# Optimization experiments

Measured on AMD Instinct MI355X. Metric: run time of the kernel, lower is better.

The kernel has to match this reference:

```python
import jax, jax.numpy as jnp
import numpy as np

INPUT_DIM, K, L, D_C = 512, 3, 512, 64
LN_EPS = 1e-5
NORM_EPS = 1e-12


def setup_inputs() -> dict:
    key = jax.random.key(0)
    ks = jax.random.split(key, 16)
    s = 0.02
    inp = {
        "x": jax.random.normal(ks[0], (65536, INPUT_DIM), jnp.float32),
        # per-sub-encoder MLP weights, stacked over K
        "W1": jax.random.normal(ks[1], (K, INPUT_DIM, 256), jnp.float32) * s,
        "b1": jnp.zeros((K, 256), jnp.float32),
        "W2": jax.random.normal(ks[2], (K, 256, 128), jnp.float32) * s,
        "b2": jnp.zeros((K, 128), jnp.float32),
        "W3": jax.random.normal(ks[3], (K, 128, D_C), jnp.float32) * s,
        "b3": jnp.zeros((K, D_C), jnp.float32),
        # shared output LayerNorm
        "gamma": jnp.ones((D_C,), jnp.float32),
        "beta": jnp.zeros((D_C,), jnp.float32),
        # codebooks: nn.Parameter(torch.randn(L, d_c)) per sub-quantizer
        "codebooks": jax.random.normal(ks[4], (K, L, D_C), jnp.float32),
        # decoder MLP d_c -> 128 -> 256 -> input_dim
        "D1": jax.random.normal(ks[5], (D_C, 128), jnp.float32) * s,
        "c1": jnp.zeros((128,), jnp.float32),
        "D2": jax.random.normal(ks[6], (128, 256), jnp.float32) * s,
        "c2": jnp.zeros((256,), jnp.float32),
        "D3": jax.random.normal(ks[7], (256, INPUT_DIM), jnp.float32) * s,
        "c3": jnp.zeros((INPUT_DIM,), jnp.float32),
    }
    return inp


def _l2norm(v, axis=-1):
    # F.normalize(p=2): x / max(||x||, eps)
    n = jnp.sqrt(jnp.sum(v * v, axis=axis, keepdims=True))
    return v / jnp.maximum(n, NORM_EPS)


def reference(x, W1, b1, W2, b2, W3, b3, gamma, beta, codebooks,
              D1, c1, D2, c2, D3, c3):
    sg = jax.lax.stop_gradient
    # encode all K sub-encoders in one batched einsum: (K, B, *)
    h = jax.nn.relu(jnp.einsum('bi,kio->kbo', x, W1) + b1[:, None, :])
    h = jax.nn.relu(jnp.einsum('kbo,kop->kbp', h, W2) + b2[:, None, :])
    enc = jnp.einsum('kbp,kpd->kbd', h, W3) + b3[:, None, :]  # (K,B,d_c)
    # LayerNorm over d_c
    mu = jnp.mean(enc, axis=-1, keepdims=True)
    var = jnp.mean((enc - mu) ** 2, axis=-1, keepdims=True)
    enc = (enc - mu) * jax.lax.rsqrt(var + LN_EPS) * gamma + beta
    # cosine quantize
    enc_n = _l2norm(enc)
    cb_n = _l2norm(codebooks)                       # (K,L,d_c)
    cos = jnp.einsum('kbd,kld->kbl', enc_n, cb_n)   # (K,B,L)
    idx = jnp.argmax(cos, axis=-1)                  # argmin(1-cos) == argmax(cos), (K,B)
    q = jnp.take_along_axis(cb_n, idx[:, :, None], axis=1)  # (K,B,d_c)
    # straight-through
    q_ste = enc + sg(q - enc)
    codebook_loss = jnp.sum(jnp.mean((sg(enc) - q_ste) ** 2, axis=(1, 2)))
    commitment_loss = jnp.sum(jnp.mean((enc - sg(q_ste)) ** 2, axis=(1, 2)))
    avg_q = jnp.mean(q_ste, axis=0)                 # (B,d_c)
    h = jax.nn.relu(avg_q @ D1 + c1)
    h = jax.nn.relu(h @ D2 + c2)
    reconstructed = h @ D3 + c3                     # (B,input_dim)
    recon_loss = jnp.mean((reconstructed - x) ** 2)
    tokens = idx.T                                  # (B,K)
    return tokens, reconstructed, recon_loss, codebook_loss, commitment_loss
```

## Files before the change

### kernel.cpp

```cpp
#include <hip/hip_runtime.h>
#include <hip/hip_bf16.h>

using f4 = float4;
typedef __attribute__((ext_vector_type(8))) short bf16x8;
typedef __attribute__((ext_vector_type(4))) float f32x4;

constexpr int IN_DIM = 512;
constexpr int DC     = 64;
constexpr int LCB    = 512;

__device__ __forceinline__ float wave_sum64(float v) {
#pragma unroll
    for (int m = 1; m < 64; m <<= 1) v += __shfl_xor(v, m, 64);
    return v;
}

__device__ __forceinline__ unsigned short f2bf(float v) {
    __hip_bfloat16 h = __float2bfloat16(v);
    return *(unsigned short*)&h;
}

__global__ void cbnorm_kernel(const float* __restrict__ cb, float* __restrict__ cbn,
                              float* __restrict__ cbnT, float* __restrict__ accv) {
    int row  = blockIdx.x * 4 + (threadIdx.x >> 6);
    int lane = threadIdx.x & 63;
    float v  = cb[(size_t)row * DC + lane];
    float ss = wave_sum64(v * v);
    float n  = sqrtf(ss);
    float o  = v / fmaxf(n, 1e-12f);
    cbn[(size_t)row * DC + lane] = o;
    int k = row >> 9, l = row & 511;
    cbnT[((size_t)k * DC + lane) * LCB + l] = o;
    if (blockIdx.x == 0 && threadIdx.x < 16) accv[threadIdx.x] = 0.f;
}

__global__ void wcvt_kernel(const float* __restrict__ D1, const float* __restrict__ D2,
                            const float* __restrict__ D3, unsigned short* __restrict__ D1t,
                            unsigned short* __restrict__ D2t, unsigned short* __restrict__ D3t) {
    int i = blockIdx.x * 256 + threadIdx.x;
    if (i < 128 * 64)  { int n = i >> 6, k = i & 63;  D1t[i] = f2bf(D1[(size_t)k * 128 + n]); }
    if (i < 256 * 128) { int n = i >> 7, k = i & 127; D2t[i] = f2bf(D2[(size_t)k * 256 + n]); }
    if (i < 512 * 256) { int n = i >> 8, k = i & 255; D3t[i] = f2bf(D3[(size_t)k * 512 + n]); }
}

__global__ void avgq_kernel(const float* __restrict__ q3, unsigned short* __restrict__ Aq,
                            int n4, size_t planeStride) {
    int i = blockIdx.x * blockDim.x + threadIdx.x;
    if (i >= n4) return;
    f4 a = *(const f4*)&q3[(size_t)i * 4];
    f4 b = *(const f4*)&q3[planeStride + (size_t)i * 4];
    f4 c = *(const f4*)&q3[2 * planeStride + (size_t)i * 4];
    const float s = 1.f / 3.f;
    unsigned int lo = f2bf((a.x + b.x + c.x) * s) | ((unsigned int)f2bf((a.y + b.y + c.y) * s) << 16);
    unsigned int hi = f2bf((a.z + b.z + c.z) * s) | ((unsigned int)f2bf((a.w + b.w + c.w) * s) << 16);
    uint2 o; o.x = lo; o.y = hi;
    *(uint2*)&Aq[(size_t)i * 4] = o;
}

template <int RELU>
__global__ __launch_bounds__(256, 4)
void gemm_kernel(const float* __restrict__ A, const float* __restrict__ W,
                 const float* __restrict__ bias, float* __restrict__ C,
                 int Kin, int N,
                 size_t aK, size_t wK, size_t bK, size_t cK) {
    constexpr int BM = 128, BN = 128, BK = 32;
    __shared__ alignas(16) float As[BK][BM + 4];
    __shared__ alignas(16) float Ws[BK][BN + 4];
    const int z = blockIdx.z;
    A += (size_t)z * aK;  W += (size_t)z * wK;
    bias += (size_t)z * bK;  C += (size_t)z * cK;
    const int tid = threadIdx.x;
    const int tx = tid & 15, ty = tid >> 4;
    const int row0 = blockIdx.x * BM, col0 = blockIdx.y * BN;

    float acc[8][8];
#pragma unroll
    for (int i = 0; i < 8; i++)
#pragma unroll
        for (int j = 0; j < 8; j++) acc[i][j] = 0.f;

    const int aRow = tid >> 3;
    const int aCol = (tid & 7) * 4;
    const int wRow = tid >> 5;
    const int wCol = (tid & 31) * 4;

    for (int kk = 0; kk < Kin; kk += BK) {
#pragma unroll
        for (int it = 0; it < 4; it++) {
            f4 v = *(const f4*)&A[(size_t)(row0 + aRow + it * 32) * Kin + kk + aCol];
            As[aCol + 0][aRow + it * 32] = v.x;
            As[aCol + 1][aRow + it * 32] = v.y;
            As[aCol + 2][aRow + it * 32] = v.z;
            As[aCol + 3][aRow + it * 32] = v.w;
        }
#pragma unroll
        for (int it = 0; it < 4; it++) {
            f4 v = *(const f4*)&W[(size_t)(kk + wRow + it * 8) * N + col0 + wCol];
            *(f4*)&Ws[wRow + it * 8][wCol] = v;
        }
        __syncthreads();
#pragma unroll
        for (int p = 0; p < BK; p++) {
            f4 a0 = *(const f4*)&As[p][ty * 8];
            f4 a1 = *(const f4*)&As[p][ty * 8 + 4];
            f4 w0 = *(const f4*)&Ws[p][tx * 8];
            f4 w1 = *(const f4*)&Ws[p][tx * 8 + 4];
            float av[8] = {a0.x, a0.y, a0.z, a0.w, a1.x, a1.y, a1.z, a1.w};
            float wv[8] = {w0.x, w0.y, w0.z, w0.w, w1.x, w1.y, w1.z, w1.w};
#pragma unroll
            for (int i = 0; i < 8; i++)
#pragma unroll
                for (int j = 0; j < 8; j++)
                    acc[i][j] = fmaf(av[i], wv[j], acc[i][j]);
        }
        __syncthreads();
    }

#pragma unroll
    for (int i = 0; i < 8; i++) {
        const size_t r = (size_t)row0 + ty * 8 + i;
        float vrow[8];
#pragma unroll
        for (int j = 0; j < 8; j++) {
            float v = acc[i][j] + bias[col0 + tx * 8 + j];
            if (RELU) v = fmaxf(v, 0.f);
            vrow[j] = v;
        }
        *(f4*)&C[r * N + col0 + tx * 8]     = *(f4*)&vrow[0];
        *(f4*)&C[r * N + col0 + tx * 8 + 4] = *(f4*)&vrow[4];
    }
}

__global__ __launch_bounds__(256, 4)
void gemm_ln_kernel(const float* __restrict__ A, const float* __restrict__ W,
                    const float* __restrict__ bias, const float* __restrict__ gamma,
                    const float* __restrict__ beta, float* __restrict__ enc, int Kin,
                    size_t aK, size_t wK, size_t bK, size_t eK) {
    constexpr int BM = 128, BK = 32;
    __shared__ alignas(16) float As[BK][BM + 4];
    __shared__ alignas(16) float Ws[BK][DC + 4];
    const int z = blockIdx.y;
    A += (size_t)z * aK;  W += (size_t)z * wK;
    bias += (size_t)z * bK;  enc += (size_t)z * eK;
    const int tid = threadIdx.x;
    const int tx = tid & 7, ty = tid >> 3;
    const int row0 = blockIdx.x * BM;

    float acc[4][8];
#pragma unroll
    for (int i = 0; i < 4; i++)
#pragma unroll
        for (int j = 0; j < 8; j++) acc[i][j] = 0.f;

    const int aRow = tid >> 3;
    const int aCol = (tid & 7) * 4;
    const int wRow = tid >> 4;
    const int wCol = (tid & 15) * 4;

    for (int kk = 0; kk < Kin; kk += BK) {
#pragma unroll
        for (int it = 0; it < 4; it++) {
            f4 v = *(const f4*)&A[(size_t)(row0 + aRow + it * 32) * Kin + kk + aCol];
            As[aCol + 0][aRow + it * 32] = v.x;
            As[aCol + 1][aRow + it * 32] = v.y;
            As[aCol + 2][aRow + it * 32] = v.z;
            As[aCol + 3][aRow + it * 32] = v.w;
        }
#pragma unroll
        for (int it = 0; it < 2; it++) {
            f4 v = *(const f4*)&W[(size_t)(kk + wRow + it * 16) * DC + wCol];
            *(f4*)&Ws[wRow + it * 16][wCol] = v;
        }
        __syncthreads();
#pragma unroll
        for (int p = 0; p < BK; p++) {
            f4 a  = *(const f4*)&As[p][ty * 4];
            f4 w0 = *(const f4*)&Ws[p][tx * 8];
            f4 w1 = *(const f4*)&Ws[p][tx * 8 + 4];
            float av[4] = {a.x, a.y, a.z, a.w};
            float wv[8] = {w0.x, w0.y, w0.z, w0.w, w1.x, w1.y, w1.z, w1.w};
#pragma unroll
            for (int i = 0; i < 4; i++)
#pragma unroll
                for (int j = 0; j < 8; j++)
                    acc[i][j] = fmaf(av[i], wv[j], acc[i][j]);
        }
        __syncthreads();
    }

#pragma unroll
    for (int i = 0; i < 4; i++) {
        float vrow[8];
#pragma unroll
        for (int j = 0; j < 8; j++) vrow[j] = acc[i][j] + bias[tx * 8 + j];
        float s = 0.f;
#pragma unroll
        for (int j = 0; j < 8; j++) s += vrow[j];
#pragma unroll
        for (int m = 1; m < 8; m <<= 1) s += __shfl_xor(s, m, 8);
        float mu = s * (1.f / 64.f);
        float d2 = 0.f;
#pragma unroll
        for (int j = 0; j < 8; j++) { float d = vrow[j] - mu; d2 = fmaf(d, d, d2); }
#pragma unroll
        for (int m = 1; m < 8; m <<= 1) d2 += __shfl_xor(d2, m, 8);
        float rs = 1.f / sqrtf(d2 * (1.f / 64.f) + 1e-5f);
#pragma unroll
        for (int j = 0; j < 8; j++) {
            int c = tx * 8 + j;
            vrow[j] = (vrow[j] - mu) * rs * gamma[c] + beta[c];
        }
        const size_t r = (size_t)row0 + ty * 4 + i;
        *(f4*)&enc[r * DC + tx * 8]     = *(f4*)&vrow[0];
        *(f4*)&enc[r * DC + tx * 8 + 4] = *(f4*)&vrow[4];
    }
}

__global__ __launch_bounds__(256, 2)
void quant_kernel(float* __restrict__ enc, const float* __restrict__ cbT,
                  const float* __restrict__ cbn, float* __restrict__ out_tok,
                  float* __restrict__ sse_acc, int row_off_glob,
                  size_t eK, size_t cbTK, size_t cbnK) {
    constexpr int BM = 128;
    __shared__ alignas(16) float Es[DC][BM + 4];
    __shared__ alignas(16) float Cs[DC][64 + 4];
    __shared__ float red[4];
    const int k = blockIdx.y;
    enc += (size_t)k * eK;
    cbT += (size_t)k * cbTK;
    cbn += (size_t)k * cbnK;
    const int tid = threadIdx.x;
    const int tx = tid & 7, ty = tid >> 3;
    const int row0 = blockIdx.x * BM;

    {
        const int r  = tid >> 1;
        const int c0 = (tid & 1) * 32;
#pragma unroll
        for (int i = 0; i < 8; i++) {
            f4 v = *(const f4*)&enc[(size_t)(row0 + r) * DC + c0 + i * 4];
            Es[c0 + i * 4 + 0][r] = v.x;
            Es[c0 + i * 4 + 1][r] = v.y;
            Es[c0 + i * 4 + 2][r] = v.z;
            Es[c0 + i * 4 + 3][r] = v.w;
        }
    }

    double mx[4]; int mi[4];
#pragma unroll
    for (int i = 0; i < 4; i++) { mx[i] = -1.0e300; mi[i] = 0; }

    for (int lc = 0; lc < LCB; lc += 64) {
        __syncthreads();
        {
            const int p  = tid >> 2;
            const int c0 = (tid & 3) * 16;
#pragma unroll
            for (int i = 0; i < 4; i++)
                *(f4*)&Cs[p][c0 + i * 4] =
                    *(const f4*)&cbT[(size_t)p * LCB + lc + c0 + i * 4];
        }
        __syncthreads();
        double sc[4][8];
#pragma unroll
        for (int i = 0; i < 4; i++)
#pragma unroll
            for (int j = 0; j < 8; j++) sc[i][j] = 0.0;
#pragma unroll
        for (int p = 0; p < DC; p++) {
            f4 a  = *(const f4*)&Es[p][ty * 4];
            f4 w0 = *(const f4*)&Cs[p][tx * 8];
            f4 w1 = *(const f4*)&Cs[p][tx * 8 + 4];
            double av[4] = {a.x, a.y, a.z, a.w};
            double wv[8] = {w0.x, w0.y, w0.z, w0.w, w1.x, w1.y, w1.z, w1.w};
#pragma unroll
            for (int i = 0; i < 4; i++)
#pragma unroll
                for (int j = 0; j < 8; j++)
                    sc[i][j] = fma(av[i], wv[j], sc[i][j]);
        }
#pragma unroll
        for (int i = 0; i < 4; i++)
#pragma unroll
            for (int j = 0; j < 8; j++) {
                int l = lc + tx * 8 + j;
                if (sc[i][j] > mx[i]) { mx[i] = sc[i][j]; mi[i] = l; }
            }
    }

#pragma unroll
    for (int m = 1; m < 8; m <<= 1)
#pragma unroll
        for (int i = 0; i < 4; i++) {
            double omx = __shfl_xor(mx[i], m, 8);
            int    omi = __shfl_xor(mi[i], m, 8);
            if (omx > mx[i] || (omx == mx[i] && omi < mi[i])) { mx[i] = omx; mi[i] = omi; }
        }

    float sse = 0.f;
#pragma unroll
    for (int i = 0; i < 4; i++) {
        const int rl = ty * 4 + i;
        const size_t r = (size_t)row0 + rl;
        f4 q0 = *(const f4*)&cbn[(size_t)mi[i] * DC + tx * 8];
        f4 q1 = *(const f4*)&cbn[(size_t)mi[i] * DC + tx * 8 + 4];
        float qv[8] = {q0.x, q0.y, q0.z, q0.w, q1.x, q1.y, q1.z, q1.w};
#pragma unroll
        for (int j = 0; j < 8; j++) {
            float e = Es[tx * 8 + j][rl];
            float d = e - qv[j];
            sse = fmaf(d, d, sse);
        }
        *(f4*)&enc[r * DC + tx * 8]     = q0;
        *(f4*)&enc[r * DC + tx * 8 + 4] = q1;
        if (tx == 0) out_tok[(size_t)(row_off_glob + r) * 3 + k] = (float)mi[i];
    }
    sse = wave_sum64(sse);
    if ((tid & 63) == 0) red[tid >> 6] = sse;
    __syncthreads();
    if (tid == 0) atomicAdd(sse_acc, red[0] + red[1] + red[2] + red[3]);
}

template <int RELU, int FINAL>
__global__ __launch_bounds__(256, 2)
void mfma_dec_kernel(const unsigned short* __restrict__ A,
                     const unsigned short* __restrict__ Wt,
                     const float* __restrict__ bias,
                     unsigned short* __restrict__ Cb, float* __restrict__ Cf,
                     const float* __restrict__ x, float* __restrict__ sse_acc,
                     int Kin, int N) {
    constexpr int BM = 128, BN = 128, BK = 32;
    __shared__ alignas(16) unsigned short As[BM][BK + 8];
    __shared__ alignas(16) unsigned short Ws[BN][BK + 8];
    __shared__ float red[4];
    const int tid = threadIdx.x;
    const int l = tid & 63, wave = tid >> 6;
    const int wr = wave >> 1, wc = wave & 1;
    const int row0 = blockIdx.x * BM, col0 = blockIdx.y * BN;

    f32x4 acc[4][4];
#pragma unroll
    for (int m = 0; m < 4; m++)
#pragma unroll
        for (int n = 0; n < 4; n++) acc[m][n] = (f32x4){0.f, 0.f, 0.f, 0.f};

    const int sRow = tid >> 1;
    const int sCol = (tid & 1) * 16;

    for (int kt = 0; kt < Kin; kt += BK) {
        __syncthreads();
        {
            uint4 a0 = *(const uint4*)&A[(size_t)(row0 + sRow) * Kin + kt + sCol];
            uint4 a1 = *(const uint4*)&A[(size_t)(row0 + sRow) * Kin + kt + sCol + 8];
            uint4 w0 = *(const uint4*)&Wt[(size_t)(col0 + sRow) * Kin + kt + sCol];
            uint4 w1 = *(const uint4*)&Wt[(size_t)(col0 + sRow) * Kin + kt + sCol + 8];
            *(uint4*)&As[sRow][sCol]     = a0;
            *(uint4*)&As[sRow][sCol + 8] = a1;
            *(uint4*)&Ws[sRow][sCol]     = w0;
            *(uint4*)&Ws[sRow][sCol + 8] = w1;
        }
        __syncthreads();
        bf16x8 af[4], bf[4];
        const int k0 = (l >> 4) * 8;
        const int lr = l & 15;
#pragma unroll
        for (int m = 0; m < 4; m++)
            af[m] = *(const bf16x8*)&As[wr * 64 + m * 16 + lr][k0];
#pragma unroll
        for (int n = 0; n < 4; n++)
            bf[n] = *(const bf16x8*)&Ws[wc * 64 + n * 16 + lr][k0];
#pragma unroll
        for (int m = 0; m < 4; m++)
#pragma unroll
            for (int n = 0; n < 4; n++)
                acc[m][n] = __builtin_amdgcn_mfma_f32_16x16x32_bf16(af[m], bf[n], acc[m][n], 0, 0, 0);
    }

    float sse = 0.f;
#pragma unroll
    for (int m = 0; m < 4; m++)
#pragma unroll
        for (int n = 0; n < 4; n++) {
            const int rbase = row0 + wr * 64 + m * 16 + (l >> 4) * 4;
            const int c = col0 + wc * 64 + n * 16 + (l & 15);
            const float b = bias[c];
#pragma unroll
            for (int rr = 0; rr < 4; rr++) {
                float v = acc[m][n][rr] + b;
                if (FINAL) {
                    float d = v - x[(size_t)(rbase + rr) * N + c];
                    sse = fmaf(d, d, sse);
                    Cf[(size_t)(rbase + rr) * N + c] = v;
                } else {
                    if (RELU) v = fmaxf(v, 0.f);
                    Cb[(size_t)(rbase + rr) * N + c] = f2bf(v);
                }
            }
        }
    if (FINAL) {
        sse = wave_sum64(sse);
        if ((tid & 63) == 0) red[tid >> 6] = sse;
        __syncthreads();
        if (tid == 0) atomicAdd(sse_acc, red[0] + red[1] + red[2] + red[3]);
    }
}

__global__ void finalize_kernel(const float* __restrict__ accv,
                                float* __restrict__ outs,
                                float inv_rec, float inv_cb) {
    if (threadIdx.x == 0) {
        outs[0] = accv[1] * inv_rec;
        float cbl = accv[0] * inv_cb;
        outs[1] = cbl;
        outs[2] = cbl;
    }
}

extern "C" void kernel_launch(void* const* d_in, const int* in_sizes, int n_in,
                              void* d_out, int out_size, void* d_ws, size_t ws_size,
                              hipStream_t stream) {
    const float* x     = (const float*)d_in[0];
    const float* W1    = (const float*)d_in[1];
    const float* b1    = (const float*)d_in[2];
    const float* W2    = (const float*)d_in[3];
    const float* b2    = (const float*)d_in[4];
    const float* W3    = (const float*)d_in[5];
    const float* b3    = (const float*)d_in[6];
    const float* gamma = (const float*)d_in[7];
    const float* beta  = (const float*)d_in[8];
    const float* cb    = (const float*)d_in[9];
    const float* D1    = (const float*)d_in[10];
    const float* c1    = (const float*)d_in[11];
    const float* D2    = (const float*)d_in[12];
    const float* c2    = (const float*)d_in[13];
    const float* D3    = (const float*)d_in[14];
    const float* c3    = (const float*)d_in[15];
    const int M = in_sizes[0] / IN_DIM;

    float* out     = (float*)d_out;
    float* out_tok = out;
    float* out_rec = out + (size_t)M * 3;
    float* out_sc  = out_rec + (size_t)M * IN_DIM;

    const size_t fixedB  = (size_t)(16 + 2 * 3 * LCB * DC) * 4 + (size_t)172032 * 2;
    const size_t perRowB = (size_t)(3 * DC + 3 * 256 + 3 * 128) * 4;
    int C = 4096;
    for (int cand = 65536; cand >= 4096; cand >>= 1)
        if (fixedB + (size_t)cand * perRowB <= ws_size) { C = cand; break; }

    float* ws    = (float*)d_ws;
    float* accv  = ws;
    float* cbn   = accv + 16;
    float* cbnT  = cbn + 3 * LCB * DC;
    unsigned short* D1t = (unsigned short*)(cbnT + 3 * DC * LCB);
    unsigned short* D2t = D1t + 128 * 64;
    unsigned short* D3t = D2t + 256 * 128;
    float* enc3  = (float*)(D3t + 512 * 256);
    float* H1    = enc3 + (size_t)3 * C * DC;
    float* H2    = H1 + (size_t)3 * C * 256;
    unsigned short* Aq  = (unsigned short*)H2;
    unsigned short* H1b = Aq + (size_t)C * 64;
    unsigned short* H2b = H1b + (size_t)C * 128;

    cbnorm_kernel<<<dim3(3 * LCB / 4), dim3(256), 0, stream>>>(cb, cbn, cbnT, accv);
    wcvt_kernel<<<dim3(512), dim3(256), 0, stream>>>(D1, D2, D3, D1t, D2t, D3t);

    for (int off = 0; off < M; off += C) {
        const float* xc  = x + (size_t)off * IN_DIM;
        float*       rcc = out_rec + (size_t)off * IN_DIM;

        gemm_kernel<1><<<dim3(C / 128, 2, 3), dim3(256), 0, stream>>>(
            xc, W1, b1, H1, 512, 256,
            0, (size_t)512 * 256, 256, (size_t)C * 256);
        gemm_kernel<1><<<dim3(C / 128, 1, 3), dim3(256), 0, stream>>>(
            H1, W2, b2, H2, 256, 128,
            (size_t)C * 256, (size_t)256 * 128, 128, (size_t)C * 128);
        gemm_ln_kernel<<<dim3(C / 128, 3), dim3(256), 0, stream>>>(
            H2, W3, b3, gamma, beta, enc3, 128,
            (size_t)C * 128, (size_t)128 * 64, 64, (size_t)C * DC);
        quant_kernel<<<dim3(C / 128, 3), dim3(256), 0, stream>>>(
            enc3, cbnT, cbn, out_tok, accv + 0, off,
            (size_t)C * DC, (size_t)DC * LCB, (size_t)LCB * DC);

        avgq_kernel<<<dim3((C * 16 + 255) / 256), dim3(256), 0, stream>>>(
            enc3, Aq, C * 16, (size_t)C * DC);
        mfma_dec_kernel<1, 0><<<dim3(C / 128, 1), dim3(256), 0, stream>>>(
            Aq, D1t, c1, H1b, nullptr, nullptr, nullptr, 64, 128);
        mfma_dec_kernel<1, 0><<<dim3(C / 128, 2), dim3(256), 0, stream>>>(
            H1b, D2t, c2, H2b, nullptr, nullptr, nullptr, 128, 256);
        mfma_dec_kernel<0, 1><<<dim3(C / 128, 4), dim3(256), 0, stream>>>(
            H2b, D3t, c3, nullptr, rcc, xc, accv + 1, 256, 512);
    }

    finalize_kernel<<<dim3(1), dim3(64), 0, stream>>>(
        accv, out_sc, 1.f / ((float)M * IN_DIM), 1.f / ((float)M * DC));
}
```

Baseline: 1.234 ms.

## Fuse encoder layer-2 GEMM into LayerNorm GEMM and prewiden codebook tile to double

```diff
diff --git a/kernel.cpp b/kernel.cpp
--- a/kernel.cpp
+++ b/kernel.cpp
@@ -132,55 +132,65 @@
 }
 
 __global__ __launch_bounds__(256, 4)
-void gemm_ln_kernel(const float* __restrict__ A, const float* __restrict__ W,
-                    const float* __restrict__ bias, const float* __restrict__ gamma,
-                    const float* __restrict__ beta, float* __restrict__ enc, int Kin,
-                    size_t aK, size_t wK, size_t bK, size_t eK) {
-    constexpr int BM = 128, BK = 32;
-    __shared__ alignas(16) float As[BK][BM + 4];
-    __shared__ alignas(16) float Ws[BK][DC + 4];
+void gemm2_ln_kernel(const float* __restrict__ A, const float* __restrict__ W2,
+                     const float* __restrict__ b2, const float* __restrict__ W3,
+                     const float* __restrict__ b3, const float* __restrict__ gamma,
+                     const float* __restrict__ beta, float* __restrict__ enc,
+                     size_t aK, size_t w2K, size_t b2K, size_t w3K, size_t b3K,
+                     size_t eK) {
+    constexpr int BM = 128, BN = 128, BK = 32, KIN = 256;
+    __shared__ union SM {
+        struct { alignas(16) float As[BK][BM + 4]; alignas(16) float Ws[BK][BN + 4]; } a;
+        struct { alignas(16) float Hs[128][66]; } b;
+    } sm;
     const int z = blockIdx.y;
-    A += (size_t)z * aK;  W += (size_t)z * wK;
-    bias += (size_t)z * bK;  enc += (size_t)z * eK;
+    A += (size_t)z * aK;
+    const float* W2p = W2 + (size_t)z * w2K;
+    const float* b2p = b2 + (size_t)z * b2K;
+    const float* W3p = W3 + (size_t)z * w3K;
+    const float* b3p = b3 + (size_t)z * b3K;
+    float* encp = enc + (size_t)z * eK;
+
     const int tid = threadIdx.x;
-    const int tx = tid & 7, ty = tid >> 3;
+    const int tx = tid & 15, ty = tid >> 4;
     const int row0 = blockIdx.x * BM;
 
-    float acc[4][8];
-#pragma unroll
-    for (int i = 0; i < 4; i++)
+    float acc[8][8];
+#pragma unroll
+    for (int i = 0; i < 8; i++)
 #pragma unroll
         for (int j = 0; j < 8; j++) acc[i][j] = 0.f;
 
     const int aRow = tid >> 3;
     const int aCol = (tid & 7) * 4;
-    const int wRow = tid >> 4;
-    const int wCol = (tid & 15) * 4;
-
-    for (int kk = 0; kk < Kin; kk += BK) {
+    const int wRow = tid >> 5;
+    const int wCol = (tid & 31) * 4;
+
+    for (int kk = 0; kk < KIN; kk += BK) {
 #pragma unroll
         for (int it = 0; it < 4; it++) {
-            f4 v = *(const f4*)&A[(size_t)(row0 + aRow + it * 32) * Kin + kk + aCol];
-            As[aCol + 0][aRow + it * 32] = v.x;
-            As[aCol + 1][aRow + it * 32] = v.y;
-            As[aCol + 2][aRow + it * 32] = v.z;
-            As[aCol + 3][aRow + it * 32] = v.w;
-        }
-#pragma unroll
-        for (int it = 0; it < 2; it++) {
-            f4 v = *(const f4*)&W[(size_t)(kk + wRow + it * 16) * DC + wCol];
-            *(f4*)&Ws[wRow + it * 16][wCol] = v;
+            f4 v = *(const f4*)&A[(size_t)(row0 + aRow + it * 32) * KIN + kk + aCol];
+            sm.a.As[aCol + 0][aRow + it * 32] = v.x;
+            sm.a.As[aCol + 1][aRow + it * 32] = v.y;
+            sm.a.As[aCol + 2][aRow + it * 32] = v.z;
+            sm.a.As[aCol + 3][aRow + it * 32] = v.w;
+        }
+#pragma unroll
+        for (int it = 0; it < 4; it++) {
+            f4 v = *(const f4*)&W2p[(size_t)(kk + wRow + it * 8) * BN + wCol];
+            *(f4*)&sm.a.Ws[wRow + it * 8][wCol] = v;
         }
         __syncthreads();
 #pragma unroll
         for (int p = 0; p < BK; p++) {
-            f4 a  = *(const f4*)&As[p][ty * 4];
-            f4 w0 = *(const f4*)&Ws[p][tx * 8];
-            f4 w1 = *(const f4*)&Ws[p][tx * 8 + 4];
-            float av[4] = {a.x, a.y, a.z, a.w};
+            f4 a0 = *(const f4*)&sm.a.As[p][ty * 8];
+            f4 a1 = *(const f4*)&sm.a.As[p][ty * 8 + 4];
+            f4 w0 = *(const f4*)&sm.a.Ws[p][tx * 8];
+            f4 w1 = *(const f4*)&sm.a.Ws[p][tx * 8 + 4];
+            float av[8] = {a0.x, a0.y, a0.z, a0.w, a1.x, a1.y, a1.z, a1.w};
             float wv[8] = {w0.x, w0.y, w0.z, w0.w, w1.x, w1.y, w1.z, w1.w};
 #pragma unroll
-            for (int i = 0; i < 4; i++)
+            for (int i = 0; i < 8; i++)
 #pragma unroll
                 for (int j = 0; j < 8; j++)
                     acc[i][j] = fmaf(av[i], wv[j], acc[i][j]);
@@ -189,30 +199,68 @@
     }
 
 #pragma unroll
-    for (int i = 0; i < 4; i++) {
-        float vrow[8];
-#pragma unroll
-        for (int j = 0; j < 8; j++) vrow[j] = acc[i][j] + bias[tx * 8 + j];
-        float s = 0.f;
-#pragma unroll
-        for (int j = 0; j < 8; j++) s += vrow[j];
-#pragma unroll
-        for (int m = 1; m < 8; m <<= 1) s += __shfl_xor(s, m, 8);
-        float mu = s * (1.f / 64.f);
-        float d2 = 0.f;
-#pragma unroll
-        for (int j = 0; j < 8; j++) { float d = vrow[j] - mu; d2 = fmaf(d, d, d2); }
-#pragma unroll
-        for (int m = 1; m < 8; m <<= 1) d2 += __shfl_xor(d2, m, 8);
-        float rs = 1.f / sqrtf(d2 * (1.f / 64.f) + 1e-5f);
-#pragma unroll
-        for (int j = 0; j < 8; j++) {
-            int c = tx * 8 + j;
-            vrow[j] = (vrow[j] - mu) * rs * gamma[c] + beta[c];
-        }
-        const size_t r = (size_t)row0 + ty * 4 + i;
-        *(f4*)&enc[r * DC + tx * 8]     = *(f4*)&vrow[0];
-        *(f4*)&enc[r * DC + tx * 8 + 4] = *(f4*)&vrow[4];
+    for (int i = 0; i < 8; i++)
+#pragma unroll
+        for (int j = 0; j < 8; j++)
+            acc[i][j] = fmaxf(acc[i][j] + b2p[tx * 8 + j], 0.f);
+
+    const int tx2 = tid & 7, ty2 = tid >> 3;
+    for (int h = 0; h < 2; ++h) {
+        if ((ty >> 3) == h) {
+            const int rbase = ty * 8 - 64 * h;
+#pragma unroll
+            for (int i = 0; i < 8; i++)
+#pragma unroll
+                for (int j = 0; j < 8; j++)
+                    sm.b.Hs[tx * 8 + j][rbase + i] = acc[i][j];
+        }
+        __syncthreads();
+
+        float acc2[2][8];
+#pragma unroll
+        for (int r = 0; r < 2; r++)
+#pragma unroll
+            for (int j = 0; j < 8; j++) acc2[r][j] = 0.f;
+
+#pragma unroll 4
+        for (int p = 0; p < 128; p++) {
+            float2 av = *(const float2*)&sm.b.Hs[p][ty2 * 2];
+            f4 w0 = *(const f4*)&W3p[(size_t)p * 64 + tx2 * 8];
+            f4 w1 = *(const f4*)&W3p[(size_t)p * 64 + tx2 * 8 + 4];
+            float wv[8] = {w0.x, w0.y, w0.z, w0.w, w1.x, w1.y, w1.z, w1.w};
+#pragma unroll
+            for (int j = 0; j < 8; j++) acc2[0][j] = fmaf(av.x, wv[j], acc2[0][j]);
+#pragma unroll
+            for (int j = 0; j < 8; j++) acc2[1][j] = fmaf(av.y, wv[j], acc2[1][j]);
+        }
+
+#pragma unroll
+        for (int r = 0; r < 2; r++) {
+            float vrow[8];
+#pragma unroll
+            for (int j = 0; j < 8; j++) vrow[j] = acc2[r][j] + b3p[tx2 * 8 + j];
+            float s = 0.f;
+#pragma unroll
+            for (int j = 0; j < 8; j++) s += vrow[j];
+#pragma unroll
+            for (int m = 1; m < 8; m <<= 1) s += __shfl_xor(s, m, 8);
+            float mu = s * (1.f / 64.f);
+            float d2 = 0.f;
+#pragma unroll
+            for (int j = 0; j < 8; j++) { float d = vrow[j] - mu; d2 = fmaf(d, d, d2); }
+#pragma unroll
+            for (int m = 1; m < 8; m <<= 1) d2 += __shfl_xor(d2, m, 8);
+            float rs = 1.f / sqrtf(d2 * (1.f / 64.f) + 1e-5f);
+#pragma unroll
+            for (int j = 0; j < 8; j++) {
+                int c = tx2 * 8 + j;
+                vrow[j] = (vrow[j] - mu) * rs * gamma[c] + beta[c];
+            }
+            const size_t rr = (size_t)row0 + 64 * h + ty2 * 2 + r;
+            *(f4*)&encp[rr * DC + tx2 * 8]     = *(f4*)&vrow[0];
+            *(f4*)&encp[rr * DC + tx2 * 8 + 4] = *(f4*)&vrow[4];
+        }
+        __syncthreads();
     }
 }
 
@@ -222,9 +270,8 @@
                   float* __restrict__ sse_acc, int row_off_glob,
                   size_t eK, size_t cbTK, size_t cbnK) {
     constexpr int BM = 128;
-    __shared__ alignas(16) float Es[DC][BM + 4];
-    __shared__ alignas(16) float Cs[DC][64 + 4];
-    __shared__ float red[4];
+    __shared__ alignas(16) float  Es[DC][BM];
+    __shared__ alignas(16) double Csd[DC][64];
     const int k = blockIdx.y;
     enc += (size_t)k * eK;
     cbT += (size_t)k * cbTK;
@@ -254,11 +301,16 @@
         __syncthreads();
         {
             const int p  = tid >> 2;
-            const int c0 = (tid & 3) * 16;
-#pragma unroll
-            for (int i = 0; i < 4; i++)
-                *(f4*)&Cs[p][c0 + i * 4] =
-                    *(const f4*)&cbT[(size_t)p * LCB + lc + c0 + i * 4];
+            const int c0 = (tid & 3) * 4;
+#pragma unroll
+            for (int i = 0; i < 4; i++) {
+                const int c = c0 + i * 16;
+                f4 v = *(const f4*)&cbT[(size_t)p * LCB + lc + c];
+                Csd[p][c + 0] = (double)v.x;
+                Csd[p][c + 1] = (double)v.y;
+                Csd[p][c + 2] = (double)v.z;
+                Csd[p][c + 3] = (double)v.w;
+            }
         }
         __syncthreads();
         double sc[4][8];
@@ -268,11 +320,13 @@
             for (int j = 0; j < 8; j++) sc[i][j] = 0.0;
 #pragma unroll
         for (int p = 0; p < DC; p++) {
-            f4 a  = *(const f4*)&Es[p][ty * 4];
-            f4 w0 = *(const f4*)&Cs[p][tx * 8];
-            f4 w1 = *(const f4*)&Cs[p][tx * 8 + 4];
+            f4 a = *(const f4*)&Es[p][ty * 4];
+            double2 w0 = *(const double2*)&Csd[p][tx * 8];
+            double2 w1 = *(const double2*)&Csd[p][tx * 8 + 2];
+            double2 w2 = *(const double2*)&Csd[p][tx * 8 + 4];
+            double2 w3 = *(const double2*)&Csd[p][tx * 8 + 6];
             double av[4] = {a.x, a.y, a.z, a.w};
-            double wv[8] = {w0.x, w0.y, w0.z, w0.w, w1.x, w1.y, w1.z, w1.w};
+            double wv[8] = {w0.x, w0.y, w1.x, w1.y, w2.x, w2.y, w3.x, w3.y};
 #pragma unroll
             for (int i = 0; i < 4; i++)
 #pragma unroll
@@ -316,6 +370,8 @@
         if (tx == 0) out_tok[(size_t)(row_off_glob + r) * 3 + k] = (float)mi[i];
     }
     sse = wave_sum64(sse);
+    __syncthreads();
+    float* red = (float*)&Es[0][0];
     if ((tid & 63) == 0) red[tid >> 6] = sse;
     __syncthreads();
     if (tid == 0) atomicAdd(sse_acc, red[0] + red[1] + red[2] + red[3]);
@@ -472,12 +528,10 @@
         gemm_kernel<1><<<dim3(C / 128, 2, 3), dim3(256), 0, stream>>>(
             xc, W1, b1, H1, 512, 256,
             0, (size_t)512 * 256, 256, (size_t)C * 256);
-        gemm_kernel<1><<<dim3(C / 128, 1, 3), dim3(256), 0, stream>>>(
-            H1, W2, b2, H2, 256, 128,
-            (size_t)C * 256, (size_t)256 * 128, 128, (size_t)C * 128);
-        gemm_ln_kernel<<<dim3(C / 128, 3), dim3(256), 0, stream>>>(
-            H2, W3, b3, gamma, beta, enc3, 128,
-            (size_t)C * 128, (size_t)128 * 64, 64, (size_t)C * DC);
+        gemm2_ln_kernel<<<dim3(C / 128, 3), dim3(256), 0, stream>>>(
+            H1, W2, b2, W3, b3, gamma, beta, enc3,
+            (size_t)C * 256, (size_t)256 * 128, 128,
+            (size_t)128 * 64, 64, (size_t)C * DC);
         quant_kernel<<<dim3(C / 128, 3), dim3(256), 0, stream>>>(
             enc3, cbnT, cbn, out_tok, accv + 0, off,
             (size_t)C * DC, (size_t)DC * LCB, (size_t)LCB * DC);
```

Result: slower. 1.302 ms (+5.5%).
